# Optimization experiments

Hardware: AMD Instinct MI355X
Metric: run time of the kernel (lower is better)

## Reference

```python
import jax, jax.numpy as jnp
import numpy as np

VOCAB, EMB, HID, OUT = 50257, 512, 1024, 5
SEQ, BATCH = 512, 64


def setup_inputs() -> dict:
    key = jax.random.key(0)
    ks = jax.random.split(key, 8)
    s_e = 1.0
    s_ih = 1.0 / np.sqrt(HID)
    return {
        "text": jax.random.randint(ks[0], (SEQ, BATCH), 0, VOCAB, dtype=jnp.int32),
        "emb": jax.random.normal(ks[1], (VOCAB, EMB), dtype=jnp.float32) * s_e,
        "W_ih": jax.random.normal(ks[2], (EMB, 3 * HID), dtype=jnp.float32) * s_ih,
        "W_hh": jax.random.normal(ks[3], (HID, 3 * HID), dtype=jnp.float32) * s_ih,
        "b_ih": jax.random.normal(ks[4], (3 * HID,), dtype=jnp.float32) * s_ih,
        "b_hh": jax.random.normal(ks[5], (3 * HID,), dtype=jnp.float32) * s_ih,
        "fc_W": jax.random.normal(ks[6], (HID, OUT), dtype=jnp.float32) * s_ih,
        "fc_b": jnp.zeros((OUT,), dtype=jnp.float32),
    }


def _gru_step(h, x_t, W_ih, W_hh, b_ih, b_hh):
    # Standard GRU cell (torch.nn.GRUCell math):
    # r = sigmoid(x Wir + bir + h Whr + bhr)
    # z = sigmoid(x Wiz + biz + h Whz + bhz)
    # h' = (1 - z) * n + z * h
    gi = x_t @ W_ih + b_ih              # [B, 3H]
    gh = h @ W_hh + b_hh                # [B, 3H]
    i_r, i_z, i_n = jnp.split(gi, 3, axis=-1)
    h_r, h_z, h_n = jnp.split(gh, 3, axis=-1)
    r = jax.nn.sigmoid(i_r + h_r)
    z = jax.nn.sigmoid(i_z + h_z)
    n = jnp.tanh(i_n + r * h_n)
    return (1.0 - z) * n + z * h


def reference(text, emb, W_ih, W_hh, b_ih, b_hh, fc_W, fc_b):
    embedded = emb[text]                # [S, B, E]
    h0 = jnp.zeros((embedded.shape[1], HID), dtype=embedded.dtype)

    def step(h, x_t):
        h_new = _gru_step(h, x_t, W_ih, W_hh, b_ih, b_hh)
        return h_new, None

    h_final, _ = jax.lax.scan(step, h0, embedded)
    return h_final @ fc_W + fc_b        # [B, OUT]
```

## Files before the change

kernel.cpp:

```cpp
#include <hip/hip_runtime.h>
#include <hip/hip_cooperative_groups.h>
#include <hip/hip_bf16.h>
#include <math.h>

constexpr int EMBD  = 512;
constexpr int HID   = 1024;
constexpr int NOUT  = 5;
constexpr int SEQ   = 512;
constexpr int BATCH = 64;

constexpr int NBLK = 64;
constexpr int NTHR = 512;
constexpr int JPB  = 16;

typedef __attribute__((ext_vector_type(8))) short bf16x8;
typedef __attribute__((ext_vector_type(4))) float f32x4;

__device__ inline unsigned short f2bf(float f) {
    __hip_bfloat16 h = __float2bfloat16(f);
    return *reinterpret_cast<unsigned short*>(&h);
}

__device__ inline bf16x8 cvt8v(f32x4 a, f32x4 b) {
    bf16x8 r;
#pragma unroll
    for (int i = 0; i < 4; i++) { __hip_bfloat16 h = __float2bfloat16(a[i]); r[i]     = *reinterpret_cast<short*>(&h); }
#pragma unroll
    for (int i = 0; i < 4; i++) { __hip_bfloat16 h = __float2bfloat16(b[i]); r[4 + i] = *reinterpret_cast<short*>(&h); }
    return r;
}

__device__ inline unsigned long long load_a8(const unsigned short* p) {
    return __hip_atomic_load((const unsigned long long*)p,
                             __ATOMIC_RELAXED, __HIP_MEMORY_SCOPE_AGENT);
}
__device__ inline void store_a8(unsigned short* p, unsigned long long v) {
    __hip_atomic_store((unsigned long long*)p, v,
                       __ATOMIC_RELAXED, __HIP_MEMORY_SCOPE_AGENT);
}
__device__ inline bf16x8 load_frag(const unsigned short* p) {
    union { unsigned long long u[2]; bf16x8 v; } r;
    r.u[0] = load_a8(p);
    r.u[1] = load_a8(p + 4);
    return r.v;
}

__device__ inline float sigm(float x) { return 1.f / (1.f + __expf(-x)); }
__device__ inline float ftanh(float x) { return 1.f - 2.f / (1.f + __expf(2.f * x)); }

__global__ __launch_bounds__(256) void pack_w(const float* __restrict__ W,
                                              unsigned short* __restrict__ out,
                                              int K) {
    const int nkt = K / 32;
    long idx = (long)blockIdx.x * 256 + threadIdx.x;
    const long total = (long)NBLK * 3 * nkt * 64;
    if (idx >= total) return;
    const int lane = idx & 63;
    long rest = idx >> 6;
    const int kt = rest % nkt; rest /= nkt;
    const int nt = rest % 3;
    const int g  = rest / 3;
    const int k0  = kt * 32 + (lane >> 4) * 8;
    const int col = nt * HID + g * JPB + (lane & 15);
    unsigned short* o = out + idx * 8;
#pragma unroll
    for (int i = 0; i < 8; i++)
        o[i] = f2bf(W[(long)(k0 + i) * 3072 + col]);
}

__global__ __launch_bounds__(256) void embed_x(const int* __restrict__ text,
                                               const float* __restrict__ emb,
                                               unsigned short* __restrict__ xfrag) {
    long idx = (long)blockIdx.x * 256 + threadIdx.x;
    if (idx >= (long)SEQ * 4 * 16 * 64) return;
    const int lane = idx & 63;
    const int kt   = (idx >> 6) & 15;
    const int bt   = (idx >> 10) & 3;
    const int t    = (int)(idx >> 12);
    const int b    = bt * 16 + (lane & 15);
    const int e0   = kt * 32 + (lane >> 4) * 8;
    const int tok  = text[t * BATCH + b];
    const float* s = emb + (long)tok * EMBD + e0;
    *(bf16x8*)(xfrag + idx * 8) = cvt8v(*(const f32x4*)s, *(const f32x4*)(s + 4));
}

__global__ void __launch_bounds__(NTHR, 2) gru_mfma(
    const unsigned short* __restrict__ xfrag,
    const float*          __restrict__ b_ih,
    const float*          __restrict__ b_hh,
    const float*          __restrict__ fc_W,
    const float*          __restrict__ fc_b,
    const unsigned short* __restrict__ whh_f,
    const unsigned short* __restrict__ wih_f,
    unsigned short*       __restrict__ hbuf,
    int*                  __restrict__ flags,
    float*                __restrict__ out)
{
    const int g    = blockIdx.x;
    const int tid  = threadIdx.x;
    const int lane = tid & 63;
    const int w    = tid >> 6;
    const int mp   = w >> 2;
    const int kq   = w & 3;
    const int l16  = lane & 15;
    const int lhi  = lane >> 4;

    __shared__ float red[8][8][256];
    __shared__ unsigned short hx[64][16];

    constexpr int HFRAG = 4 * 32 * 64 * 8;

    for (int i = tid; i < 512; i += NTHR)
        store_a8(hbuf + ((long)g * 512 + i) * 4, 0ull);

    const int jg = g * JPB + l16;
    const float bir  = b_ih[jg],           bhr = b_hh[jg];
    const float biz  = b_ih[HID + jg],     bhz = b_hh[HID + jg];
    const float bin_ = b_ih[2 * HID + jg], bhn = b_hh[2 * HID + jg];

    const bool gateW  = (kq < 2);
    const bool storeW = (kq >= 2);
    const int  mtG    = mp * 2 + kq;
    const int  mtS    = mp * 2 + (kq - 2);
    float hp[4] = {0.f, 0.f, 0.f, 0.f};

    bf16x8 xa0[4], xa1[4];
    auto loadX = [&](int t) {
        const unsigned short* base = xfrag + (long)t * (4 * 16 * 64 * 8);
#pragma unroll
        for (int kk = 0; kk < 4; kk++) {
            const int kt = kq * 4 + kk;
            xa0[kk] = *(const bf16x8*)(base + (((2 * mp + 0) * 16 + kt) * 64 + lane) * 8);
            xa1[kk] = *(const bf16x8*)(base + (((2 * mp + 1) * 16 + kt) * 64 + lane) * 8);
        }
    };

    const int sb  = mtS * 16 + ((lane >> 1) & 15);
    const int sjl = ((lane >> 1) >> 4) * 8 + 4 * (lane & 1);
    const long sdst = (((long)mtS * 32 + (g >> 1)) * 64) * 8 + 256 * (g & 1) + lane * 4;

    const unsigned short* whh_g = whh_f + (long)g * 3 * 32 * 64 * 8;
    const unsigned short* wih_g = wih_f + (long)g * 3 * 16 * 64 * 8;

    asm volatile("s_waitcnt vmcnt(0)" ::: "memory");
    __syncthreads();
    if (tid == 0)
        __hip_atomic_store(&flags[g], 1, __ATOMIC_RELAXED, __HIP_MEMORY_SCOPE_AGENT);
    loadX(0);
    if (tid < 64) {
        int f = __hip_atomic_load(&flags[tid], __ATOMIC_RELAXED, __HIP_MEMORY_SCOPE_AGENT);
        while (__any(f < 1)) {
            __builtin_amdgcn_s_sleep(2);
            f = __hip_atomic_load(&flags[tid], __ATOMIC_RELAXED, __HIP_MEMORY_SCOPE_AGENT);
        }
    }
    __syncthreads();

    for (int t = 0; t < SEQ; ++t) {
        const unsigned short* hr = hbuf + (long)(t & 1) * HFRAG;
        unsigned short*       hw = hbuf + (long)((t + 1) & 1) * HFRAG;

        bf16x8 ha0[8], ha1[8];
#pragma unroll
        for (int kk = 0; kk < 8; kk++) {
            const int kt = kq * 8 + kk;
            ha0[kk] = load_frag(hr + (((long)(2 * mp + 0) * 32 + kt) * 64 + lane) * 8);
            ha1[kk] = load_frag(hr + (((long)(2 * mp + 1) * 32 + kt) * 64 + lane) * 8);
        }

        f32x4 aR0 = {0,0,0,0}, aR1 = {0,0,0,0};
        f32x4 aZ0 = {0,0,0,0}, aZ1 = {0,0,0,0};
        f32x4 aGh0 = {0,0,0,0}, aGh1 = {0,0,0,0};
        f32x4 aGi0 = {0,0,0,0}, aGi1 = {0,0,0,0};

#pragma unroll
        for (int kk = 0; kk < 4; kk++) {
            const unsigned short* bp = wih_g + (((long)(kq * 4 + kk)) * 64 + lane) * 8;
            const bf16x8 bR = *(const bf16x8*)(bp);
            const bf16x8 bZ = *(const bf16x8*)(bp + 16 * 64 * 8);
            const bf16x8 bN = *(const bf16x8*)(bp + 2 * 16 * 64 * 8);
            aR0  = __builtin_amdgcn_mfma_f32_16x16x32_bf16(xa0[kk], bR, aR0, 0, 0, 0);
            aR1  = __builtin_amdgcn_mfma_f32_16x16x32_bf16(xa1[kk], bR, aR1, 0, 0, 0);
            aZ0  = __builtin_amdgcn_mfma_f32_16x16x32_bf16(xa0[kk], bZ, aZ0, 0, 0, 0);
            aZ1  = __builtin_amdgcn_mfma_f32_16x16x32_bf16(xa1[kk], bZ, aZ1, 0, 0, 0);
            aGi0 = __builtin_amdgcn_mfma_f32_16x16x32_bf16(xa0[kk], bN, aGi0, 0, 0, 0);
            aGi1 = __builtin_amdgcn_mfma_f32_16x16x32_bf16(xa1[kk], bN, aGi1, 0, 0, 0);
        }

#pragma unroll
        for (int kk = 0; kk < 8; kk++) {
            const int kt = kq * 8 + kk;
            const unsigned short* bp = whh_g + (((long)kt) * 64 + lane) * 8;
            const bf16x8 bR = *(const bf16x8*)(bp);
            const bf16x8 bZ = *(const bf16x8*)(bp + 32 * 64 * 8);
            const bf16x8 bN = *(const bf16x8*)(bp + 2 * 32 * 64 * 8);
            aR0  = __builtin_amdgcn_mfma_f32_16x16x32_bf16(ha0[kk], bR, aR0, 0, 0, 0);
            aR1  = __builtin_amdgcn_mfma_f32_16x16x32_bf16(ha1[kk], bR, aR1, 0, 0, 0);
            aZ0  = __builtin_amdgcn_mfma_f32_16x16x32_bf16(ha0[kk], bZ, aZ0, 0, 0, 0);
            aZ1  = __builtin_amdgcn_mfma_f32_16x16x32_bf16(ha1[kk], bZ, aZ1, 0, 0, 0);
            aGh0 = __builtin_amdgcn_mfma_f32_16x16x32_bf16(ha0[kk], bN, aGh0, 0, 0, 0);
            aGh1 = __builtin_amdgcn_mfma_f32_16x16x32_bf16(ha1[kk], bN, aGh1, 0, 0, 0);
        }

        *(f32x4*)&red[w][0][lane * 4] = aR0;
        *(f32x4*)&red[w][1][lane * 4] = aR1;
        *(f32x4*)&red[w][2][lane * 4] = aZ0;
        *(f32x4*)&red[w][3][lane * 4] = aZ1;
        *(f32x4*)&red[w][4][lane * 4] = aGh0;
        *(f32x4*)&red[w][5][lane * 4] = aGh1;
        *(f32x4*)&red[w][6][lane * 4] = aGi0;
        *(f32x4*)&red[w][7][lane * 4] = aGi1;
        __syncthreads();

        if (gateW) {
            const int s = kq;
            f32x4 R  = {0,0,0,0}, Z = {0,0,0,0}, Gh = {0,0,0,0}, Gi = {0,0,0,0};
#pragma unroll
            for (int q = 0; q < 4; q++) {
                const int src = mp * 4 + q;
                R  += *(const f32x4*)&red[src][0 + s][lane * 4];
                Z  += *(const f32x4*)&red[src][2 + s][lane * 4];
                Gh += *(const f32x4*)&red[src][4 + s][lane * 4];
                Gi += *(const f32x4*)&red[src][6 + s][lane * 4];
            }
#pragma unroll
            for (int r = 0; r < 4; r++) {
                const float rr = sigm(R[r] + bir + bhr);
                const float zz = sigm(Z[r] + biz + bhz);
                const float nn = ftanh(Gi[r] + bin_ + rr * (Gh[r] + bhn));
                const float hn = (1.f - zz) * nn + zz * hp[r];
                hp[r] = hn;
                hx[mtG * 16 + lhi * 4 + r][l16] = f2bf(hn);
            }
        }
        __syncthreads();

        if (storeW) {
            const unsigned long long v =
                *(const unsigned long long*)&hx[sb][sjl];
            store_a8(hw + sdst, v);
            asm volatile("s_waitcnt vmcnt(0)" ::: "memory");
        }
        __syncthreads();

        if (tid == 0)
            __hip_atomic_store(&flags[g], t + 2, __ATOMIC_RELAXED, __HIP_MEMORY_SCOPE_AGENT);
        loadX((t + 1 < SEQ) ? t + 1 : SEQ - 1);
        if (tid < 64) {
            int f = __hip_atomic_load(&flags[tid], __ATOMIC_RELAXED, __HIP_MEMORY_SCOPE_AGENT);
            while (__any(f < t + 2)) {
                __builtin_amdgcn_s_sleep(2);
                f = __hip_atomic_load(&flags[tid], __ATOMIC_RELAXED, __HIP_MEMORY_SCOPE_AGENT);
            }
        }
        __syncthreads();
    }

    float (*hsl)[JPB] = reinterpret_cast<float(*)[JPB]>(&red[0][0][0]);
    if (gateW) {
#pragma unroll
        for (int r = 0; r < 4; r++) {
            const int b = mtG * 16 + lhi * 4 + r;
            hsl[b][l16] = hp[r];
        }
    }
    __syncthreads();
    if (tid < BATCH * NOUT) {
        const int b = tid / NOUT, o = tid - b * NOUT;
        float acc = (g == 0) ? fc_b[o] : 0.0f;
#pragma unroll
        for (int jl = 0; jl < JPB; jl++)
            acc += hsl[b][jl] * fc_W[(g * JPB + jl) * NOUT + o];
        atomicAdd(&out[tid], acc);
    }
}

extern "C" void kernel_launch(void* const* d_in, const int* in_sizes, int n_in,
                              void* d_out, int out_size, void* d_ws, size_t ws_size,
                              hipStream_t stream) {
    const int*   text = (const int*)  d_in[0];
    const float* emb  = (const float*)d_in[1];
    const float* W_ih = (const float*)d_in[2];
    const float* W_hh = (const float*)d_in[3];
    const float* b_ih = (const float*)d_in[4];
    const float* b_hh = (const float*)d_in[5];
    const float* fc_W = (const float*)d_in[6];
    const float* fc_b = (const float*)d_in[7];
    float* out = (float*)d_out;

    char* ws = (char*)d_ws;
    int*            flags = (int*)(ws);
    unsigned short* hbuf  = (unsigned short*)(ws + 4096);
    unsigned short* whh_f = (unsigned short*)(ws + 4096 + 262144);
    unsigned short* wih_f = (unsigned short*)(ws + 4096 + 262144 + 6291456);
    unsigned short* xfrag = (unsigned short*)(ws + 4096 + 262144 + 6291456 + 3145728);

    hipMemsetAsync(flags, 0, 4096, stream);
    hipMemsetAsync(out, 0, (size_t)out_size * sizeof(float), stream);

    const long nfrag_hh = (long)NBLK * 3 * 32 * 64;
    const long nfrag_ih = (long)NBLK * 3 * 16 * 64;
    pack_w<<<(int)((nfrag_hh + 255) / 256), 256, 0, stream>>>(W_hh, whh_f, HID);
    pack_w<<<(int)((nfrag_ih + 255) / 256), 256, 0, stream>>>(W_ih, wih_f, EMBD);

    const long nx = (long)SEQ * 4 * 16 * 64;
    embed_x<<<(int)((nx + 255) / 256), 256, 0, stream>>>(text, emb, xfrag);

    void* args[] = { (void*)&xfrag, (void*)&b_ih, (void*)&b_hh,
                     (void*)&fc_W, (void*)&fc_b, (void*)&whh_f, (void*)&wih_f,
                     (void*)&hbuf, (void*)&flags, (void*)&out };
    hipLaunchCooperativeKernel((void*)gru_mfma, dim3(NBLK), dim3(NTHR), args, 0, stream);
}
```

Before: 3.041 ms.

## Merge gate and store phases to drop a barrier, prefetch next x early

The gate-computing waves now write their own h fragment to global memory straight after computing it, which removes one __syncthreads per timestep. Each wave's own partial accumulators are used directly and only the other waves' partials are read from LDS. The next timestep's x fragments are loaded into double-buffered registers earlier in the step, the hx row is padded, and the spin-wait sleep is shortened. This adds register pressure and concentrates the global store latency on the gate waves.

```diff
diff --git a/kernel.cpp b/kernel.cpp
--- a/kernel.cpp
+++ b/kernel.cpp
@@ -106,7 +106,7 @@
     const int lhi  = lane >> 4;
 
     __shared__ float red[8][8][256];
-    __shared__ unsigned short hx[64][16];
+    __shared__ unsigned short hx[64][20];
 
     constexpr int HFRAG = 4 * 32 * 64 * 8;
 
@@ -118,26 +118,24 @@
     const float biz  = b_ih[HID + jg],     bhz = b_hh[HID + jg];
     const float bin_ = b_ih[2 * HID + jg], bhn = b_hh[2 * HID + jg];
 
-    const bool gateW  = (kq < 2);
-    const bool storeW = (kq >= 2);
-    const int  mtG    = mp * 2 + kq;
-    const int  mtS    = mp * 2 + (kq - 2);
+    const bool gateW = (kq < 2);
+    const int  mtG   = mp * 2 + kq;
     float hp[4] = {0.f, 0.f, 0.f, 0.f};
 
-    bf16x8 xa0[4], xa1[4];
-    auto loadX = [&](int t) {
+    bf16x8 xa0[4], xa1[4], xb0[4], xb1[4];
+    auto loadX = [&](int t, bf16x8 (&d0)[4], bf16x8 (&d1)[4]) {
         const unsigned short* base = xfrag + (long)t * (4 * 16 * 64 * 8);
 #pragma unroll
         for (int kk = 0; kk < 4; kk++) {
             const int kt = kq * 4 + kk;
-            xa0[kk] = *(const bf16x8*)(base + (((2 * mp + 0) * 16 + kt) * 64 + lane) * 8);
-            xa1[kk] = *(const bf16x8*)(base + (((2 * mp + 1) * 16 + kt) * 64 + lane) * 8);
+            d0[kk] = *(const bf16x8*)(base + (((2 * mp + 0) * 16 + kt) * 64 + lane) * 8);
+            d1[kk] = *(const bf16x8*)(base + (((2 * mp + 1) * 16 + kt) * 64 + lane) * 8);
         }
     };
 
-    const int sb  = mtS * 16 + ((lane >> 1) & 15);
-    const int sjl = ((lane >> 1) >> 4) * 8 + 4 * (lane & 1);
-    const long sdst = (((long)mtS * 32 + (g >> 1)) * 64) * 8 + 256 * (g & 1) + lane * 4;
+    const int sb2  = mtG * 16 + ((lane >> 1) & 15);
+    const int sjl2 = ((lane >> 1) >> 4) * 8 + 4 * (lane & 1);
+    const long sdstG = (((long)mtG * 32 + (g >> 1)) * 64) * 8 + 256 * (g & 1) + lane * 4;
 
     const unsigned short* whh_g = whh_f + (long)g * 3 * 32 * 64 * 8;
     const unsigned short* wih_g = wih_f + (long)g * 3 * 16 * 64 * 8;
@@ -146,11 +144,11 @@
     __syncthreads();
     if (tid == 0)
         __hip_atomic_store(&flags[g], 1, __ATOMIC_RELAXED, __HIP_MEMORY_SCOPE_AGENT);
-    loadX(0);
+    loadX(0, xa0, xa1);
     if (tid < 64) {
         int f = __hip_atomic_load(&flags[tid], __ATOMIC_RELAXED, __HIP_MEMORY_SCOPE_AGENT);
         while (__any(f < 1)) {
-            __builtin_amdgcn_s_sleep(2);
+            __builtin_amdgcn_s_sleep(1);
             f = __hip_atomic_load(&flags[tid], __ATOMIC_RELAXED, __HIP_MEMORY_SCOPE_AGENT);
         }
     }
@@ -159,6 +157,7 @@
     for (int t = 0; t < SEQ; ++t) {
         const unsigned short* hr = hbuf + (long)(t & 1) * HFRAG;
         unsigned short*       hw = hbuf + (long)((t + 1) & 1) * HFRAG;
+        const int tn = (t + 1 < SEQ) ? t + 1 : SEQ - 1;
 
         bf16x8 ha0[8], ha1[8];
 #pragma unroll
@@ -167,6 +166,8 @@
             ha0[kk] = load_frag(hr + (((long)(2 * mp + 0) * 32 + kt) * 64 + lane) * 8);
             ha1[kk] = load_frag(hr + (((long)(2 * mp + 1) * 32 + kt) * 64 + lane) * 8);
         }
+        __builtin_amdgcn_sched_barrier(0);
+        if (!gateW) loadX(tn, xb0, xb1);
 
         f32x4 aR0 = {0,0,0,0}, aR1 = {0,0,0,0};
         f32x4 aZ0 = {0,0,0,0}, aZ1 = {0,0,0,0};
@@ -214,9 +215,13 @@
 
         if (gateW) {
             const int s = kq;
-            f32x4 R  = {0,0,0,0}, Z = {0,0,0,0}, Gh = {0,0,0,0}, Gi = {0,0,0,0};
+            f32x4 R  = (s == 0) ? aR0  : aR1;
+            f32x4 Z  = (s == 0) ? aZ0  : aZ1;
+            f32x4 Gh = (s == 0) ? aGh0 : aGh1;
+            f32x4 Gi = (s == 0) ? aGi0 : aGi1;
 #pragma unroll
             for (int q = 0; q < 4; q++) {
+                if (q == kq) continue;
                 const int src = mp * 4 + q;
                 R  += *(const f32x4*)&red[src][0 + s][lane * 4];
                 Z  += *(const f32x4*)&red[src][2 + s][lane * 4];
@@ -232,28 +237,28 @@
                 hp[r] = hn;
                 hx[mtG * 16 + lhi * 4 + r][l16] = f2bf(hn);
             }
-        }
-        __syncthreads();
-
-        if (storeW) {
-            const unsigned long long v =
-                *(const unsigned long long*)&hx[sb][sjl];
-            store_a8(hw + sdst, v);
+            asm volatile("s_waitcnt lgkmcnt(0)" ::: "memory");
+            __builtin_amdgcn_sched_barrier(0);
+            const unsigned long long v = *(const unsigned long long*)&hx[sb2][sjl2];
+            store_a8(hw + sdstG, v);
             asm volatile("s_waitcnt vmcnt(0)" ::: "memory");
+            loadX(tn, xb0, xb1);
         }
         __syncthreads();
 
         if (tid == 0)
             __hip_atomic_store(&flags[g], t + 2, __ATOMIC_RELAXED, __HIP_MEMORY_SCOPE_AGENT);
-        loadX((t + 1 < SEQ) ? t + 1 : SEQ - 1);
         if (tid < 64) {
             int f = __hip_atomic_load(&flags[tid], __ATOMIC_RELAXED, __HIP_MEMORY_SCOPE_AGENT);
             while (__any(f < t + 2)) {
-                __builtin_amdgcn_s_sleep(2);
+                __builtin_amdgcn_s_sleep(1);
                 f = __hip_atomic_load(&flags[tid], __ATOMIC_RELAXED, __HIP_MEMORY_SCOPE_AGENT);
             }
         }
         __syncthreads();
+
+#pragma unroll
+        for (int kk = 0; kk < 4; kk++) { xa0[kk] = xb0[kk]; xa1[kk] = xb1[kk]; }
     }
 
     float (*hsl)[JPB] = reinterpret_cast<float(*)[JPB]>(&red[0][0][0]);
```

After: 6.922 ms. 2.28x slower.
